# Kernel tuning notes

Hardware: AMD Instinct MI355X
Metric: run time of the kernel (lower is better)

Reference implementation:

```python
import jax, jax.numpy as jnp
import numpy as np

# Module constants (match init_kwargs)
M = 2049                      # NpointsMesh (odd)
TAU = 2.821e-5                # Gaussian spreading width ~ 12*(pi/M)^2
XLIMS = (0.0, 10.0)
L = abs(XLIMS[1] - XLIMS[0])
KGRID = jnp.asarray(np.linspace(-(M // 2), M // 2, M), dtype=jnp.float32)        # (M,)
XGRID = jnp.asarray(2.0 * np.pi * np.linspace(XLIMS[0], XLIMS[1], M + 1)[:-1] / L,
                    dtype=jnp.float32)                                           # (M,)
FOUR_PI = 4.0 * np.pi


def setup_inputs() -> dict:
    key = jax.random.key(0)
    kx, = jax.random.split(key, 1)
    x = jax.random.uniform(kx, (16, 1024), dtype=jnp.float32) * 10.0  # points in [xLims[0], xLims[1])
    ones = jnp.ones((1,), dtype=jnp.float32)  # tf.initializers.ones for all 4 weights
    return {"x": x, "shift0": ones, "amp0": ones, "shift1": ones, "amp1": ones}


def reference(x, shift0, amp0, shift1, amp1):
    # Gaussian spreading: (B, N, M)
    diff = x[..., None] * (2.0 * np.pi / L) - XGRID
    g = jnp.exp(-jnp.square(diff) / (4.0 * TAU))
    # Sum over points -> gridded density (B, M), then FFT + shift
    gsum = jnp.sum(g, axis=1).astype(jnp.complex64)
    fft_g = jnp.fft.fftshift(jnp.fft.fft(gsum, axis=-1), axes=-1) * (L / (2.0 * np.pi))
    # Deconvolution of the Gaussian kernel (real-valued)
    deconv = jnp.sqrt(np.pi / TAU) * jnp.exp(jnp.square(KGRID) * TAU)  # (M,)
    rfft = fft_g * deconv  # (B, M) complex
    # Fourier multipliers (real; imag parts are structurally zero in the original)
    m1 = -amp0 * FOUR_PI / (jnp.square(KGRID) + jnp.square(5.0 * shift0))            # (M,)
    m2 = amp1 * FOUR_PI * jnp.square(1.0 / (jnp.square(KGRID) + jnp.square(5.0 * shift1)))  # (M,)
    mult = jnp.stack([m1, m2], axis=0)  # (2, M)
    mult_fft = mult[None, :, :].astype(jnp.complex64) * rfft[:, None, :]  # (B, 2, M)
    mult_deconv = mult_fft * deconv  # second deconv application, as in the original
    # Inverse FFT back to the mesh, keep real part: (B, 2, M)
    irfft = jnp.real(jnp.fft.ifft(jnp.fft.ifftshift(mult_deconv, axes=-1), axis=-1))
    # Inverse interpolation back to the points: (B, N, 2, M) -> (B, N, 2)
    local = irfft[:, None, :, :] * g[:, :, None, :]
    fmm = jnp.sum(local, axis=-1) / M
    return fmm
```

## Files before the change

kernel.cpp:

```cpp
#include <hip/hip_runtime.h>
#include <math.h>

#define M_   2049
#define B_   16
#define N_   1024
#define TAU_ 2.821e-5
#define PI_  3.14159265358979323846
#define TWO_PI_ 6.283185307179586476925286766559

#define GS_CH    8
#define H_JSPLIT 16
#define CV_SPLIT 16
#define FMM_LPP  16
#define MPAD     2052

#define SW(i) ((i) + ((i) >> 2))

__global__ void spread_h_kernel(const float* __restrict__ x,
                                const float* __restrict__ s0, const float* __restrict__ a0,
                                const float* __restrict__ s1, const float* __restrict__ a1,
                                double* __restrict__ gpart, double* __restrict__ hpart) {
    __shared__ double smem[M_ + 128];
    const int bx = blockIdx.x;

    if (bx < GS_CH * B_) {
        const int b  = bx / GS_CH;
        const int ch = bx % GS_CH;
        for (int i = threadIdx.x; i < M_; i += 256) smem[i] = 0.0;
        __syncthreads();
        const int pl  = threadIdx.x >> 1;
        const int sub = threadIdx.x & 1;
        const double du      = TWO_PI_ / (double)M_;
        const double inv4tau = 1.0 / (4.0 * TAU_);
        const double u = (double)x[b * N_ + ch * (N_ / GS_CH) + pl] * (TWO_PI_ / 10.0);
        const int mc = (int)(u / du + 0.5);
        const int start = mc - 33 + sub * 34;
        for (int i = 0; i < 34; ++i) {
            int m = start + i;
            if (m >= 0 && m < M_) {
                double d = u - du * (double)m;
                double t = d * d * inv4tau;
                if (t < 88.0) atomicAdd(&smem[m], (double)__expf(-(float)t));
            }
        }
        __syncthreads();
        double* gp = gpart + ((size_t)ch * B_ + b) * M_;
        for (int i = threadIdx.x; i < M_; i += 256) gp[i] = smem[i];
    } else {
        const int t  = bx - GS_CH * B_;
        const int dt = t % 5;
        const int jc = t / 5;
        double* costab = smem;
        double* cf0    = smem + M_;
        double* cf1    = smem + M_ + 64;
        const int jlo = 1 + jc * (1024 / H_JSPLIT);
        const double ang0 = TWO_PI_ / (double)M_;

        for (int i = threadIdx.x; i <= 1024; i += 256) {
            double v = cos(ang0 * (double)i);
            costab[i] = v;
            if (i > 0) costab[M_ - i] = v;
        }
        if (threadIdx.x < 1024 / H_JSPLIT) {
            int j = jlo + threadIdx.x;
            double k2   = (double)j * (double)j;
            double dec2 = (PI_ / TAU_) * exp(2.0 * TAU_ * k2);
            double base = 2.0 * (10.0 / TWO_PI_) * dec2 / (double)M_;
            double sA = 5.0 * (double)s0[0];
            cf0[threadIdx.x] = base * (-(double)a0[0] * 4.0 * PI_ / (k2 + sA * sA));
            double sB = 5.0 * (double)s1[0];
            double den = k2 + sB * sB;
            cf1[threadIdx.x] = base * ((double)a1[0] * 4.0 * PI_ / (den * den));
        }
        __syncthreads();

        const int d = dt * 256 + threadIdx.x;
        if (d > 1024) return;

        double acc0 = 0.0, acc1 = 0.0;
        if (jc == 0) {
            double w0base = (10.0 / TWO_PI_) * (PI_ / TAU_) / (double)M_;
            double sA = 5.0 * (double)s0[0];
            acc0 = w0base * (-(double)a0[0] * 4.0 * PI_ / (sA * sA));
            double sB = 5.0 * (double)s1[0];
            acc1 = w0base * ((double)a1[0] * 4.0 * PI_ / ((sB * sB) * (sB * sB)));
        }
        int r = (int)(((long long)jlo * (long long)d) % M_);
        #pragma unroll 4
        for (int jj = 0; jj < 1024 / H_JSPLIT; ++jj) {
            double cv_ = costab[r];
            acc0 += cf0[jj] * cv_;
            acc1 += cf1[jj] * cv_;
            r += d; if (r >= M_) r -= M_;
        }
        double* hp = hpart + (size_t)jc * 2050;
        hp[d]        = acc0;
        hp[1025 + d] = acc1;
    }
}

__global__ void gred_kernel(const double* __restrict__ gpart, const double* __restrict__ hpart,
                            double* __restrict__ gsum, double* __restrict__ hhalf) {
    const int idx = blockIdx.x * 256 + threadIdx.x;
    if (idx < B_ * M_) {
        const size_t sstride = (size_t)B_ * M_;
        double acc = 0.0;
        #pragma unroll
        for (int k = 0; k < GS_CH; ++k) acc += gpart[(size_t)k * sstride + idx];
        gsum[idx] = acc;
    } else if (idx < B_ * M_ + 2050) {
        const int e = idx - B_ * M_;
        double acc = 0.0;
        #pragma unroll
        for (int k = 0; k < H_JSPLIT; ++k) acc += hpart[(size_t)k * 2050 + e];
        hhalf[e] = acc;
    }
}

__global__ void conv_kernel(const double* __restrict__ gsum, const double* __restrict__ hhalf,
                            double* __restrict__ part) {
    __shared__ double w0s[1456];
    __shared__ double w1s[1456];
    __shared__ double red[512];
    const int mt = blockIdx.x;
    const int s  = blockIdx.y;
    const int b  = blockIdx.z;
    const int m0  = mt * 1024;
    const int p0  = (s * M_) / CV_SPLIT;
    const int p1  = ((s + 1) * M_) / CV_SPLIT;
    const int len = p1 - p0;
    const int wcount = 1024 + len;
    int base = m0 - (p0 + len - 1);
    while (base < 0) base += M_;
    for (int i = threadIdx.x; i < wcount; i += 256) {
        int idx = base + i;
        while (idx >= M_) idx -= M_;
        int d = (idx > 1024) ? (M_ - idx) : idx;
        w0s[SW(i)] = hhalf[d];
        w1s[SW(i)] = hhalf[1025 + d];
    }
    __syncthreads();

    const double* gs = gsum + (size_t)b * M_ + p0;

    int q = 4 * threadIdx.x + len - 1;
    double c0w0 = w0s[SW(q)],   c0w1 = w0s[SW(q+1)], c0w2 = w0s[SW(q+2)], c0w3 = w0s[SW(q+3)];
    double c1w0 = w1s[SW(q)],   c1w1 = w1s[SW(q+1)], c1w2 = w1s[SW(q+2)], c1w3 = w1s[SW(q+3)];
    double a00 = 0.0, a01 = 0.0, a02 = 0.0, a03 = 0.0;
    double a10 = 0.0, a11 = 0.0, a12 = 0.0, a13 = 0.0;
    #pragma unroll 4
    for (int t = 0; t < len; ++t) {
        double g = gs[t];
        a00 += g * c0w0; a01 += g * c0w1; a02 += g * c0w2; a03 += g * c0w3;
        a10 += g * c1w0; a11 += g * c1w1; a12 += g * c1w2; a13 += g * c1w3;
        c0w3 = c0w2; c0w2 = c0w1; c0w1 = c0w0;
        c1w3 = c1w2; c1w2 = c1w1; c1w1 = c1w0;
        --q;
        c0w0 = w0s[SW(q)]; c1w0 = w1s[SW(q)];
    }
    {
        double* pv = part + (((size_t)s * B_ + b) * 2) * MPAD + m0 + 4 * threadIdx.x;
        pv[0]        = a00; pv[1]        = a01; pv[2]        = a02; pv[3]        = a03;
        pv[MPAD + 0] = a10; pv[MPAD + 1] = a11; pv[MPAD + 2] = a12; pv[MPAD + 3] = a13;
    }

    if (mt == 1) {
        double t0 = 0.0, t1 = 0.0;
        if (threadIdx.x < len) {
            double g = gs[threadIdx.x];
            int qq = 1023 + len - threadIdx.x;
            t0 = g * w0s[SW(qq)];
            t1 = g * w1s[SW(qq)];
        }
        red[threadIdx.x]       = t0;
        red[256 + threadIdx.x] = t1;
        __syncthreads();
        for (int off = 128; off > 0; off >>= 1) {
            if (threadIdx.x < off) {
                red[threadIdx.x]       += red[threadIdx.x + off];
                red[256 + threadIdx.x] += red[256 + threadIdx.x + off];
            }
            __syncthreads();
        }
        if (threadIdx.x == 0) {
            double* pv = part + (((size_t)s * B_ + b) * 2) * MPAD;
            pv[2048]        = red[0];
            pv[MPAD + 2048] = red[256];
        }
    }
}

__global__ void reduce_kernel(const double* __restrict__ part, double* __restrict__ conv) {
    const int idx = blockIdx.x * 256 + threadIdx.x;
    if (idx >= B_ * 2 * M_) return;
    const int b  = idx / (2 * M_);
    const int rm = idx - b * 2 * M_;
    const int c  = rm / M_;
    const int m  = rm - c * M_;
    const size_t off = ((size_t)b * 2 + c) * MPAD + m;
    const size_t sstride = (size_t)B_ * 2 * MPAD;
    double acc = 0.0;
    #pragma unroll
    for (int k = 0; k < CV_SPLIT; ++k)
        acc += part[(size_t)k * sstride + off];
    conv[idx] = acc;
}

__global__ void fmm_kernel(const float* __restrict__ x, const double* __restrict__ conv,
                           float* __restrict__ out) {
    const int gid = blockIdx.x * 256 + threadIdx.x;
    const int pt  = gid / FMM_LPP;
    const int sub = gid % FMM_LPP;
    const int b   = pt >> 10;
    const double du      = TWO_PI_ / (double)M_;
    const double inv4tau = 1.0 / (4.0 * TAU_);
    const double u = (double)x[pt] * (TWO_PI_ / 10.0);
    int mc = (int)(u / du + 0.5);
    int lo = mc - 34; if (lo < 0) lo = 0;
    int hi = mc + 34; if (hi > M_ - 1) hi = M_ - 1;
    const double* c0 = conv + (size_t)(b * 2) * M_;
    const double* c1 = c0 + M_;
    double a0 = 0.0, a1 = 0.0;
    for (int m = lo + sub; m <= hi; m += FMM_LPP) {
        double d = u - du * (double)m;
        double g = (double)__expf(-(float)(d * d * inv4tau));
        a0 += g * c0[m];
        a1 += g * c1[m];
    }
    a0 += __shfl_xor(a0, 1); a1 += __shfl_xor(a1, 1);
    a0 += __shfl_xor(a0, 2); a1 += __shfl_xor(a1, 2);
    a0 += __shfl_xor(a0, 4); a1 += __shfl_xor(a1, 4);
    a0 += __shfl_xor(a0, 8); a1 += __shfl_xor(a1, 8);
    if (sub == 0) {
        out[pt * 2 + 0] = (float)(a0 / (double)M_);
        out[pt * 2 + 1] = (float)(a1 / (double)M_);
    }
}

extern "C" void kernel_launch(void* const* d_in, const int* in_sizes, int n_in,
                              void* d_out, int out_size, void* d_ws, size_t ws_size,
                              hipStream_t stream) {
    (void)in_sizes; (void)n_in; (void)out_size; (void)ws_size;
    const float* x  = (const float*)d_in[0];
    const float* s0 = (const float*)d_in[1];
    const float* a0 = (const float*)d_in[2];
    const float* s1 = (const float*)d_in[3];
    const float* a1 = (const float*)d_in[4];
    float* out = (float*)d_out;

    double* gsum  = (double*)d_ws;
    double* hhalf = gsum + B_ * M_;
    double* conv  = hhalf + 2 * 1025;
    double* part  = conv + B_ * 2 * M_;
    double* gpart = part + (size_t)CV_SPLIT * B_ * 2 * MPAD;
    double* hpart = gpart + (size_t)GS_CH * B_ * M_;

    hipLaunchKernelGGL(spread_h_kernel, dim3(GS_CH * B_ + 5 * H_JSPLIT), dim3(256), 0,
                       stream, x, s0, a0, s1, a1, gpart, hpart);
    hipLaunchKernelGGL(gred_kernel, dim3((B_ * M_ + 2050 + 255) / 256), dim3(256), 0,
                       stream, gpart, hpart, gsum, hhalf);
    hipLaunchKernelGGL(conv_kernel, dim3(2, CV_SPLIT, B_), dim3(256), 0, stream,
                       gsum, hhalf, part);
    hipLaunchKernelGGL(reduce_kernel, dim3((B_ * 2 * M_ + 255) / 256), dim3(256), 0, stream,
                       part, conv);
    hipLaunchKernelGGL(fmm_kernel, dim3(B_ * N_ * FMM_LPP / 256), dim3(256), 0, stream,
                       x, conv, out);
}
```

Before: 91.97 us.

## Fuse partial reduction into FMM kernel, use cosine recurrence, halve split counts

Removes the separate reduce kernel: each FMM block sums the convolution partials for its batch into shared float memory and then interpolates 256 points from there. The H-kernel cosine table is replaced by a Chebyshev three-term recurrence per output, and the j and convolution split factors drop from 16 to 8, with shared buffers and the wrap-around reduction loop resized to match. This saves a launch and a global round-trip, but each batch's reduction is redone by four blocks, the FMM grid shrinks to 64 blocks, and the interpolation now runs partly in float instead of double.

```diff
diff --git a/kernel.cpp b/kernel.cpp
--- a/kernel.cpp
+++ b/kernel.cpp
@@ -9,27 +9,28 @@
 #define TWO_PI_ 6.283185307179586476925286766559
 
 #define GS_CH    8
-#define H_JSPLIT 16
-#define CV_SPLIT 16
-#define FMM_LPP  16
+#define H_JSPLIT 8
+#define CV_SPLIT 8
 #define MPAD     2052
 
 #define SW(i) ((i) + ((i) >> 2))
+
 
 __global__ void spread_h_kernel(const float* __restrict__ x,
                                 const float* __restrict__ s0, const float* __restrict__ a0,
                                 const float* __restrict__ s1, const float* __restrict__ a1,
                                 double* __restrict__ gpart, double* __restrict__ hpart) {
-    __shared__ double smem[M_ + 128];
-    const int bx = blockIdx.x;
+    __shared__ double smem[M_ + 64];
+    const int bx  = blockIdx.x;
+    const int tid = threadIdx.x;
 
     if (bx < GS_CH * B_) {
         const int b  = bx / GS_CH;
         const int ch = bx % GS_CH;
-        for (int i = threadIdx.x; i < M_; i += 256) smem[i] = 0.0;
-        __syncthreads();
-        const int pl  = threadIdx.x >> 1;
-        const int sub = threadIdx.x & 1;
+        for (int i = tid; i < M_; i += 256) smem[i] = 0.0;
+        __syncthreads();
+        const int pl  = tid >> 1;
+        const int sub = tid & 1;
         const double du      = TWO_PI_ / (double)M_;
         const double inv4tau = 1.0 / (4.0 * TAU_);
         const double u = (double)x[b * N_ + ch * (N_ / GS_CH) + pl] * (TWO_PI_ / 10.0);
@@ -45,57 +46,51 @@
         }
         __syncthreads();
         double* gp = gpart + ((size_t)ch * B_ + b) * M_;
-        for (int i = threadIdx.x; i < M_; i += 256) gp[i] = smem[i];
+        for (int i = tid; i < M_; i += 256) gp[i] = smem[i];
     } else {
         const int t  = bx - GS_CH * B_;
         const int dt = t % 5;
         const int jc = t / 5;
-        double* costab = smem;
-        double* cf0    = smem + M_;
-        double* cf1    = smem + M_ + 64;
-        const int jlo = 1 + jc * (1024 / H_JSPLIT);
-        const double ang0 = TWO_PI_ / (double)M_;
-
-        for (int i = threadIdx.x; i <= 1024; i += 256) {
-            double v = cos(ang0 * (double)i);
-            costab[i] = v;
-            if (i > 0) costab[M_ - i] = v;
-        }
-        if (threadIdx.x < 1024 / H_JSPLIT) {
-            int j = jlo + threadIdx.x;
+        const int jlo = 1 + jc * 128;
+        double* cf0 = smem;
+        double* cf1 = smem + 128;
+        const double sA = 5.0 * (double)s0[0];
+        const double sB = 5.0 * (double)s1[0];
+        const double A0 = -(double)a0[0] * 4.0 * PI_;
+        const double A1 =  (double)a1[0] * 4.0 * PI_;
+        if (tid < 128) {
+            int j = jlo + tid;
             double k2   = (double)j * (double)j;
             double dec2 = (PI_ / TAU_) * exp(2.0 * TAU_ * k2);
             double base = 2.0 * (10.0 / TWO_PI_) * dec2 / (double)M_;
-            double sA = 5.0 * (double)s0[0];
-            cf0[threadIdx.x] = base * (-(double)a0[0] * 4.0 * PI_ / (k2 + sA * sA));
-            double sB = 5.0 * (double)s1[0];
+            cf0[tid] = base * (A0 / (k2 + sA * sA));
             double den = k2 + sB * sB;
-            cf1[threadIdx.x] = base * ((double)a1[0] * 4.0 * PI_ / (den * den));
-        }
-        __syncthreads();
-
-        const int d = dt * 256 + threadIdx.x;
-        if (d > 1024) return;
-
-        double acc0 = 0.0, acc1 = 0.0;
-        if (jc == 0) {
-            double w0base = (10.0 / TWO_PI_) * (PI_ / TAU_) / (double)M_;
-            double sA = 5.0 * (double)s0[0];
-            acc0 = w0base * (-(double)a0[0] * 4.0 * PI_ / (sA * sA));
-            double sB = 5.0 * (double)s1[0];
-            acc1 = w0base * ((double)a1[0] * 4.0 * PI_ / ((sB * sB) * (sB * sB)));
-        }
-        int r = (int)(((long long)jlo * (long long)d) % M_);
-        #pragma unroll 4
-        for (int jj = 0; jj < 1024 / H_JSPLIT; ++jj) {
-            double cv_ = costab[r];
-            acc0 += cf0[jj] * cv_;
-            acc1 += cf1[jj] * cv_;
-            r += d; if (r >= M_) r -= M_;
-        }
-        double* hp = hpart + (size_t)jc * 2050;
-        hp[d]        = acc0;
-        hp[1025 + d] = acc1;
+            cf1[tid] = base * (A1 / (den * den));
+        }
+        __syncthreads();
+        const int d = dt * 256 + tid;
+        if (d <= 1024) {
+            double acc0 = 0.0, acc1 = 0.0;
+            if (jc == 0) {
+                double w0base = (10.0 / TWO_PI_) * (PI_ / TAU_) / (double)M_;
+                acc0 = w0base * (A0 / (sA * sA));
+                acc1 = w0base * (A1 / ((sB * sB) * (sB * sB)));
+            }
+            const double theta = TWO_PI_ * (double)d / (double)M_;
+            const double twoc1 = 2.0 * cos(theta);
+            double cm1 = cos((double)(jlo - 1) * theta);
+            double c   = cos((double)jlo * theta);
+            #pragma unroll 4
+            for (int jj = 0; jj < 128; ++jj) {
+                acc0 += cf0[jj] * c;
+                acc1 += cf1[jj] * c;
+                double cn = fma(twoc1, c, -cm1);
+                cm1 = c; c = cn;
+            }
+            double* hp = hpart + (size_t)jc * 2050;
+            hp[d]        = acc0;
+            hp[1025 + d] = acc1;
+        }
     }
 }
 
@@ -119,8 +114,8 @@
 
 __global__ void conv_kernel(const double* __restrict__ gsum, const double* __restrict__ hhalf,
                             double* __restrict__ part) {
-    __shared__ double w0s[1456];
-    __shared__ double w1s[1456];
+    __shared__ double w0s[1604];
+    __shared__ double w1s[1604];
     __shared__ double red[512];
     const int mt = blockIdx.x;
     const int s  = blockIdx.y;
@@ -163,14 +158,13 @@
         pv[0]        = a00; pv[1]        = a01; pv[2]        = a02; pv[3]        = a03;
         pv[MPAD + 0] = a10; pv[MPAD + 1] = a11; pv[MPAD + 2] = a12; pv[MPAD + 3] = a13;
     }
-
     if (mt == 1) {
         double t0 = 0.0, t1 = 0.0;
-        if (threadIdx.x < len) {
-            double g = gs[threadIdx.x];
-            int qq = 1023 + len - threadIdx.x;
-            t0 = g * w0s[SW(qq)];
-            t1 = g * w1s[SW(qq)];
+        for (int mp = threadIdx.x; mp < len; mp += 256) {
+            double g = gs[mp];
+            int qq = 1023 + len - mp;
+            t0 += g * w0s[SW(qq)];
+            t1 += g * w1s[SW(qq)];
         }
         red[threadIdx.x]       = t0;
         red[256 + threadIdx.x] = t1;
@@ -190,50 +184,51 @@
     }
 }
 
-__global__ void reduce_kernel(const double* __restrict__ part, double* __restrict__ conv) {
-    const int idx = blockIdx.x * 256 + threadIdx.x;
-    if (idx >= B_ * 2 * M_) return;
-    const int b  = idx / (2 * M_);
-    const int rm = idx - b * 2 * M_;
-    const int c  = rm / M_;
-    const int m  = rm - c * M_;
-    const size_t off = ((size_t)b * 2 + c) * MPAD + m;
+__global__ void fmm_kernel(const float* __restrict__ x, const double* __restrict__ part,
+                           float* __restrict__ out) {
+    __shared__ float cf[2 * M_];
+    const int b  = blockIdx.x >> 2;
+    const int pc = blockIdx.x & 3;
+    const int tid = threadIdx.x;
     const size_t sstride = (size_t)B_ * 2 * MPAD;
-    double acc = 0.0;
-    #pragma unroll
-    for (int k = 0; k < CV_SPLIT; ++k)
-        acc += part[(size_t)k * sstride + off];
-    conv[idx] = acc;
-}
-
-__global__ void fmm_kernel(const float* __restrict__ x, const double* __restrict__ conv,
-                           float* __restrict__ out) {
-    const int gid = blockIdx.x * 256 + threadIdx.x;
-    const int pt  = gid / FMM_LPP;
-    const int sub = gid % FMM_LPP;
-    const int b   = pt >> 10;
+    for (int i = tid; i < 2 * M_; i += 256) {
+        const int c = (i >= M_) ? 1 : 0;
+        const int m = i - c * M_;
+        const size_t off = ((size_t)b * 2 + c) * MPAD + m;
+        double acc = 0.0;
+        #pragma unroll
+        for (int k = 0; k < CV_SPLIT; ++k)
+            acc += part[(size_t)k * sstride + off];
+        cf[i] = (float)acc;
+    }
+    __syncthreads();
+
+    const int sub = tid & 15;
+    const int pl  = tid >> 4;
     const double du      = TWO_PI_ / (double)M_;
     const double inv4tau = 1.0 / (4.0 * TAU_);
-    const double u = (double)x[pt] * (TWO_PI_ / 10.0);
-    int mc = (int)(u / du + 0.5);
-    int lo = mc - 34; if (lo < 0) lo = 0;
-    int hi = mc + 34; if (hi > M_ - 1) hi = M_ - 1;
-    const double* c0 = conv + (size_t)(b * 2) * M_;
-    const double* c1 = c0 + M_;
-    double a0 = 0.0, a1 = 0.0;
-    for (int m = lo + sub; m <= hi; m += FMM_LPP) {
-        double d = u - du * (double)m;
-        double g = (double)__expf(-(float)(d * d * inv4tau));
-        a0 += g * c0[m];
-        a1 += g * c1[m];
-    }
-    a0 += __shfl_xor(a0, 1); a1 += __shfl_xor(a1, 1);
-    a0 += __shfl_xor(a0, 2); a1 += __shfl_xor(a1, 2);
-    a0 += __shfl_xor(a0, 4); a1 += __shfl_xor(a1, 4);
-    a0 += __shfl_xor(a0, 8); a1 += __shfl_xor(a1, 8);
-    if (sub == 0) {
-        out[pt * 2 + 0] = (float)(a0 / (double)M_);
-        out[pt * 2 + 1] = (float)(a1 / (double)M_);
+    #pragma unroll 2
+    for (int pass = 0; pass < 16; ++pass) {
+        const int pt = b * N_ + pc * 256 + pass * 16 + pl;
+        const double u = (double)x[pt] * (TWO_PI_ / 10.0);
+        int mc = (int)(u / du + 0.5);
+        int lo = mc - 34; if (lo < 0) lo = 0;
+        int hi = mc + 34; if (hi > M_ - 1) hi = M_ - 1;
+        double a0v = 0.0, a1v = 0.0;
+        for (int m = lo + sub; m <= hi; m += 16) {
+            double d = u - du * (double)m;
+            float g = __expf(-(float)(d * d * inv4tau));
+            a0v += (double)(g * cf[m]);
+            a1v += (double)(g * cf[M_ + m]);
+        }
+        a0v += __shfl_xor(a0v, 1); a1v += __shfl_xor(a1v, 1);
+        a0v += __shfl_xor(a0v, 2); a1v += __shfl_xor(a1v, 2);
+        a0v += __shfl_xor(a0v, 4); a1v += __shfl_xor(a1v, 4);
+        a0v += __shfl_xor(a0v, 8); a1v += __shfl_xor(a1v, 8);
+        if (sub == 0) {
+            out[pt * 2 + 0] = (float)(a0v / (double)M_);
+            out[pt * 2 + 1] = (float)(a1v / (double)M_);
+        }
     }
 }
 
@@ -250,8 +245,7 @@
 
     double* gsum  = (double*)d_ws;
     double* hhalf = gsum + B_ * M_;
-    double* conv  = hhalf + 2 * 1025;
-    double* part  = conv + B_ * 2 * M_;
+    double* part  = hhalf + 2 * 1025;
     double* gpart = part + (size_t)CV_SPLIT * B_ * 2 * MPAD;
     double* hpart = gpart + (size_t)GS_CH * B_ * M_;
 
@@ -261,8 +255,6 @@
                        stream, gpart, hpart, gsum, hhalf);
     hipLaunchKernelGGL(conv_kernel, dim3(2, CV_SPLIT, B_), dim3(256), 0, stream,
                        gsum, hhalf, part);
-    hipLaunchKernelGGL(reduce_kernel, dim3((B_ * 2 * M_ + 255) / 256), dim3(256), 0, stream,
-                       part, conv);
-    hipLaunchKernelGGL(fmm_kernel, dim3(B_ * N_ * FMM_LPP / 256), dim3(256), 0, stream,
-                       x, conv, out);
-}
+    hipLaunchKernelGGL(fmm_kernel, dim3(B_ * 4), dim3(256), 0, stream,
+                       x, part, out);
+}
```

Result: slower. 113.9 us (+23.9%).
